# Performance work log

Hardware: AMD Instinct MI355X
Metric: run time of the kernel (lower is better)

The kernel has to match this reference:

```python
import jax, jax.numpy as jnp
import numpy as np

N, E, IN_DIM, HID, HEADS, LAYERS, NUM_STORES = 50000, 800000, 64, 128, 16, 3, 50
DH = HID // HEADS  # per-head dim = 8
EPS = 1e-5


def setup_inputs() -> dict:
    key = jax.random.key(0)
    ks = iter(jax.random.split(key, 40))
    def nrm(shape, scale):
        return jax.random.normal(next(ks), shape, dtype=jnp.float32) * scale
    inp = {}
    inp['x'] = jax.random.normal(next(ks), (N, IN_DIM), dtype=jnp.float32)
    inp['edge_index'] = jax.random.randint(next(ks), (2, E), 0, N, dtype=jnp.int32)
    inp['edge_weight'] = jax.random.uniform(next(ks), (E, 1), dtype=jnp.float32)
    inp['store_mask'] = jax.random.randint(next(ks), (N,), 0, NUM_STORES, dtype=jnp.int32)
    # input_proj: Linear + GELU + LayerNorm
    inp['in_W'] = nrm((IN_DIM, HID), IN_DIM ** -0.5)
    inp['in_b'] = jnp.zeros((HID,), jnp.float32)
    inp['in_g'] = jnp.ones((HID,), jnp.float32)
    inp['in_beta'] = jnp.zeros((HID,), jnp.float32)
    # 3 stacked GATv2 layers (stacked leading dim = layer)
    s = HID ** -0.5
    inp['gat_Wl'] = nrm((LAYERS, HID, HID), s)
    inp['gat_bl'] = jnp.zeros((LAYERS, HID), jnp.float32)
    inp['gat_Wr'] = nrm((LAYERS, HID, HID), s)
    inp['gat_br'] = jnp.zeros((LAYERS, HID), jnp.float32)
    inp['gat_We'] = nrm((LAYERS, 1, HID), 1.0)
    inp['gat_att'] = nrm((LAYERS, HEADS, DH), DH ** -0.5)
    inp['gat_bias'] = jnp.zeros((LAYERS, HID), jnp.float32)
    inp['blk_g'] = jnp.ones((LAYERS, HID), jnp.float32)
    inp['blk_b'] = jnp.zeros((LAYERS, HID), jnp.float32)
    # per-store context gate + final norm
    inp['ctx_W'] = nrm((HID, HID), s)
    inp['ctx_b'] = jnp.zeros((HID,), jnp.float32)
    inp['fin_g'] = jnp.ones((HID,), jnp.float32)
    inp['fin_b'] = jnp.zeros((HID,), jnp.float32)
    return inp


def layernorm(x, g, b):
    mu = jnp.mean(x, axis=-1, keepdims=True)
    v = jnp.mean((x - mu) ** 2, axis=-1, keepdims=True)
    return (x - mu) * jax.lax.rsqrt(v + EPS) * g + b


def gatv2_layer(x, src, dst, ea, Wl, bl, Wr, br, We, att, bias):
    # x: [N, HID]; src/dst: [Et]; ea: [Et, 1]
    n = x.shape[0]
    xl = (x @ Wl + bl).reshape(n, HEADS, DH)   # source transform
    xr = (x @ Wr + br).reshape(n, HEADS, DH)   # target transform
    ee = (ea @ We).reshape(-1, HEADS, DH)      # edge-attr embedding
    e = jax.nn.leaky_relu(xl[src] + xr[dst] + ee, 0.2)  # [Et, H, D]
    logit = jnp.einsum('ehd,hd->eh', e, att)             # [Et, H]
    # segment softmax over incoming edges of each target node
    mx = jax.ops.segment_max(logit, dst, num_segments=n)
    p = jnp.exp(logit - mx[dst])
    Z = jax.ops.segment_sum(p, dst, num_segments=n)
    alpha = p / (Z[dst] + 1e-16)
    msg = alpha[:, :, None] * xl[src]                    # [Et, H, D]
    agg = jax.ops.segment_sum(msg, dst, num_segments=n)  # [N, H, D]
    return agg.reshape(n, HEADS * DH) + bias


def forward(x, edge_index, edge_weight, store_mask, in_W, in_b, in_g, in_beta,
            gat_Wl, gat_bl, gat_Wr, gat_br, gat_We, gat_att, gat_bias,
            blk_g, blk_b, ctx_W, ctx_b, fin_g, fin_b):
    n = x.shape[0]
    h = layernorm(jax.nn.gelu(x @ in_W + in_b, approximate=False), in_g, in_beta)
    src, dst = edge_index[0], edge_index[1]
    # PyG add_self_loops with fill_value='mean': per-target mean of incoming edge attrs
    deg = jax.ops.segment_sum(jnp.ones(src.shape, h.dtype), dst, num_segments=n)
    loop_attr = jax.ops.segment_sum(edge_weight, dst, num_segments=n) / jnp.maximum(deg, 1.0)[:, None]
    loops = jnp.arange(n, dtype=src.dtype)
    srcf = jnp.concatenate([src, loops])
    dstf = jnp.concatenate([dst, loops])
    eaf = jnp.concatenate([edge_weight, loop_attr], axis=0)
    for l in range(LAYERS):  # residual block: post-norm residual around conv
        m = gatv2_layer(h, srcf, dstf, eaf, gat_Wl[l], gat_bl[l], gat_Wr[l], gat_br[l],
                        gat_We[l], gat_att[l], gat_bias[l])
        h = layernorm(h + m, blk_g[l], blk_b[l])
    # per-store segmented mean -> sigmoid gate -> scatter back
    cnt = jax.ops.segment_sum(jnp.ones((n,), h.dtype), store_mask, num_segments=NUM_STORES)
    means = jax.ops.segment_sum(h, store_mask, num_segments=NUM_STORES) / jnp.maximum(cnt, 1.0)[:, None]
    gate = jax.nn.sigmoid(means @ ctx_W + ctx_b)
    h = h + (gate * means)[store_mask]
    return layernorm(h, fin_g, fin_b)


def reference(x, edge_index, edge_weight, store_mask, in_W, in_b, in_g, in_beta,
              gat_Wl, gat_bl, gat_Wr, gat_br, gat_We, gat_att, gat_bias,
              blk_g, blk_b, ctx_W, ctx_b, fin_g, fin_b):
    return forward(x, edge_index, edge_weight, store_mask, in_W, in_b, in_g, in_beta,
                   gat_Wl, gat_bl, gat_Wr, gat_br, gat_We, gat_att, gat_bias,
                   blk_g, blk_b, ctx_W, ctx_b, fin_g, fin_b)
```

## Files before the change

kernel.cpp:

```cpp
#include <hip/hip_runtime.h>
#include <math.h>

#define NN 50000
#define EE 800000
#define ET (EE + NN)
#define HID 128
#define NSTORE 50
#define NBL 196
#define CVT_B 12500
#define CNT_B 3125
#define SCT_B 3321
#define GEMB 391
#define SSB 512

typedef unsigned short ushort_t;
typedef unsigned long long u64;
typedef __attribute__((ext_vector_type(8))) short bf8;
typedef __attribute__((ext_vector_type(4))) float f4;
typedef __attribute__((ext_vector_type(4))) unsigned int u4;

__device__ __forceinline__ float b2f(ushort_t u) {
    union { unsigned int i; float f; } v; v.i = ((unsigned int)u) << 16; return v.f;
}
__device__ __forceinline__ ushort_t f2b(float f) {
    union { float f; unsigned int i; } v; v.f = f;
    unsigned int r = (v.i + 0x7fffu + ((v.i >> 16) & 1u)) >> 16;
    return (ushort_t)r;
}
__device__ __forceinline__ void b2f2(unsigned int u, float& lo, float& hi) {
    union { unsigned int i; float f; } a, c;
    a.i = u << 16; c.i = u & 0xffff0000u;
    lo = a.f; hi = c.f;
}
__device__ __forceinline__ unsigned int pk2(float lo, float hi) {
    return (unsigned int)f2b(lo) | ((unsigned int)f2b(hi) << 16);
}

__global__ __launch_bounds__(256) void k_build(const float* __restrict__ x, const float* __restrict__ inW,
                                               const float* __restrict__ gWl, const float* __restrict__ gWr,
                                               const int* __restrict__ ei, const float* __restrict__ ew,
                                               ushort_t* __restrict__ xb, ushort_t* __restrict__ inWt,
                                               ushort_t* __restrict__ Wlt, ushort_t* __restrict__ Wrt,
                                               u64* __restrict__ packed, int* __restrict__ rank) {
    int b = blockIdx.x, t = threadIdx.x;
    if (b < CVT_B) {
        int i = b * 256 + t;
        xb[i] = f2b(x[i]);
        if (i < 128 * 64) {
            int c = i >> 6, k = i & 63;
            inWt[i] = f2b(inW[k * 128 + c]);
        }
        if (i < 3 * 128 * 128) {
            int l = i >> 14, r = i & 16383, nn2 = r >> 7, k = r & 127;
            Wlt[i] = f2b(gWl[(size_t)l * 16384 + k * 128 + nn2]);
            Wrt[i] = f2b(gWr[(size_t)l * 16384 + k * 128 + nn2]);
        }
    } else {
        int i = (b - CVT_B) * 256 + t;
        if (i < EE) {
            int dst = ei[EE + i];
            unsigned int wfix = __float2uint_rn(ew[i] * 16777216.0f);
            u64 old = atomicAdd(&packed[dst], (1ULL << 44) | (u64)wfix);
            rank[i] = (int)(old >> 44);
        }
    }
}

__global__ __launch_bounds__(256) void k_psum(const u64* __restrict__ packed, int* __restrict__ bsum) {
    int t = threadIdx.x, bidx = blockIdx.x;
    int i = bidx * 256 + t;
    int v = (i < NN) ? (int)(packed[i] >> 44) + 1 : 0;
#pragma unroll
    for (int d = 1; d < 64; d <<= 1) v += __shfl_xor(v, d);
    __shared__ int ws4[4];
    if ((t & 63) == 0) ws4[t >> 6] = v;
    __syncthreads();
    if (t == 0) bsum[bidx] = ws4[0] + ws4[1] + ws4[2] + ws4[3];
}

__global__ __launch_bounds__(256) void k_scanb(const int* __restrict__ bsum,
                                               int* __restrict__ bbase, int* __restrict__ offs) {
    __shared__ int s[256];
    int t = threadIdx.x;
    int v = (t < NBL) ? bsum[t] : 0;
    s[t] = v;
    __syncthreads();
    for (int d = 1; d < 256; d <<= 1) {
        int u = (t >= d) ? s[t - d] : 0;
        __syncthreads();
        s[t] += u;
        __syncthreads();
    }
    if (t < NBL) bbase[t] = s[t] - v;
    if (t == 0) offs[NN] = ET;
}

__global__ __launch_bounds__(256) void k_offs(const u64* __restrict__ packed,
                                              const int* __restrict__ bbase, int* __restrict__ offs) {
    __shared__ int wsum4[4];
    int t = threadIdx.x, bidx = blockIdx.x;
    int i = bidx * 256 + t;
    int v = (i < NN) ? (int)(packed[i] >> 44) + 1 : 0;
    int lane = t & 63, w = t >> 6;
    int sc = v;
#pragma unroll
    for (int d = 1; d < 64; d <<= 1) {
        int u = __shfl_up(sc, d);
        if (lane >= d) sc += u;
    }
    if (lane == 63) wsum4[w] = sc;
    __syncthreads();
    int wo = 0;
    for (int k = 0; k < w; ++k) wo += wsum4[k];
    if (i < NN) offs[i] = bbase[bidx] + wo + sc - v;
}

__global__ __launch_bounds__(256) void k_inproj(const ushort_t* __restrict__ A,
                                                const ushort_t* __restrict__ Wt,
                                                const float* __restrict__ bias,
                                                const float* __restrict__ g,
                                                const float* __restrict__ be,
                                                float* __restrict__ h,
                                                ushort_t* __restrict__ hb) {
    const int K = 64;
    __shared__ float s1[2][128], s2[2][128];
    int lane = threadIdx.x & 63, w = threadIdx.x >> 6;
    int rw = w >> 1, cw = w & 1;
    int q = lane >> 4, l16 = lane & 15;
    int row0 = blockIdx.x * 128 + rw * 64;
    int col0 = cw * 64;
    bf8 z; for (int t = 0; t < 8; ++t) z[t] = 0;

    bf8 bfr[2][4];
#pragma unroll
    for (int kk = 0; kk < 2; ++kk)
#pragma unroll
        for (int j = 0; j < 4; ++j)
            bfr[kk][j] = *(const bf8*)(Wt + (size_t)(col0 + j * 16 + l16) * K + kk * 32 + q * 8);

    f4 acc[4][4];
#pragma unroll
    for (int i = 0; i < 4; ++i)
#pragma unroll
        for (int j = 0; j < 4; ++j) acc[i][j] = (f4)(0.f);

#pragma unroll
    for (int kk = 0; kk < 2; ++kk) {
        bf8 af[4];
#pragma unroll
        for (int i = 0; i < 4; ++i) {
            int r = row0 + i * 16 + l16;
            af[i] = (r < NN) ? *(const bf8*)(A + (size_t)r * K + kk * 32 + q * 8) : z;
        }
#pragma unroll
        for (int i = 0; i < 4; ++i)
#pragma unroll
            for (int j = 0; j < 4; ++j)
                acc[i][j] = __builtin_amdgcn_mfma_f32_16x16x32_bf16(af[i], bfr[kk][j], acc[i][j], 0, 0, 0);
    }
#pragma unroll
    for (int i = 0; i < 4; ++i) {
#pragma unroll
        for (int j = 0; j < 4; ++j) {
            float bv = bias[col0 + j * 16 + l16];
#pragma unroll
            for (int r = 0; r < 4; ++r) {
                float v = acc[i][j][r] + bv;
                v = 0.5f * v * (1.f + erff(v * 0.70710678118654752f));
                acc[i][j][r] = v;
            }
        }
    }
#pragma unroll
    for (int i = 0; i < 4; ++i) {
#pragma unroll
        for (int r = 0; r < 4; ++r) {
            float sm = acc[i][0][r] + acc[i][1][r] + acc[i][2][r] + acc[i][3][r];
            float sq = acc[i][0][r] * acc[i][0][r] + acc[i][1][r] * acc[i][1][r]
                     + acc[i][2][r] * acc[i][2][r] + acc[i][3][r] * acc[i][3][r];
#pragma unroll
            for (int k = 1; k < 16; k <<= 1) { sm += __shfl_xor(sm, k); sq += __shfl_xor(sq, k); }
            if (l16 == 0) {
                int rl = rw * 64 + i * 16 + q * 4 + r;
                s1[cw][rl] = sm; s2[cw][rl] = sq;
            }
        }
    }
    __syncthreads();
#pragma unroll
    for (int i = 0; i < 4; ++i) {
#pragma unroll
        for (int r = 0; r < 4; ++r) {
            int rl = rw * 64 + i * 16 + q * 4 + r;
            int gr = blockIdx.x * 128 + rl;
            if (gr >= NN) continue;
            float sm = s1[0][rl] + s1[1][rl];
            float sq = s2[0][rl] + s2[1][rl];
            float mu = sm * (1.f / 128.f);
            float var = sq * (1.f / 128.f) - mu * mu;
            float rinv = rsqrtf(var + 1e-5f);
#pragma unroll
            for (int j = 0; j < 4; ++j) {
                int gc = col0 + j * 16 + l16;
                float v = (acc[i][j][r] - mu) * rinv * g[gc] + be[gc];
                h[(size_t)gr * HID + gc] = v;
                hb[(size_t)gr * HID + gc] = f2b(v);
            }
        }
    }
}

__global__ __launch_bounds__(256) void k_gemm2(const ushort_t* __restrict__ A,
                                               const ushort_t* __restrict__ Wt0,
                                               const ushort_t* __restrict__ Wt1,
                                               const float* __restrict__ b0,
                                               const float* __restrict__ b1,
                                               ushort_t* __restrict__ o0,
                                               ushort_t* __restrict__ o1, int n,
                                               const int* __restrict__ ei,
                                               const float* __restrict__ ew,
                                               const int* __restrict__ offs,
                                               const u64* __restrict__ packed,
                                               const int* __restrict__ rank,
                                               int2* __restrict__ csr) {
    int bid = blockIdx.x;
    if (bid >= 2 * GEMB) {
        int i = (bid - 2 * GEMB) * 256 + threadIdx.x;
        if (i < EE) {
            int src = ei[i], dst = ei[EE + i];
            int pos = offs[dst] + rank[i];
            int2 v; v.x = src; v.y = __float_as_int(ew[i]);
            csr[pos] = v;
        } else if (i < ET) {
            int nd = i - EE;
            u64 p = packed[nd];
            int deg = (int)(p >> 44);
            float wsf = (float)(p & ((1ULL << 44) - 1)) * (1.0f / 16777216.0f);
            float la = wsf / fmaxf((float)deg, 1.0f);
            int pos = offs[nd + 1] - 1;
            int2 v; v.x = nd; v.y = __float_as_int(la);
            csr[pos] = v;
        }
        return;
    }
    const int K = 128;
    int by = (bid >= GEMB) ? 1 : 0;
    int bx = by ? bid - GEMB : bid;
    const ushort_t* Wt = by ? Wt1 : Wt0;
    const float* bias = by ? b1 : b0;
    ushort_t* outb = by ? o1 : o0;
    int lane = threadIdx.x & 63, w = threadIdx.x >> 6;
    int rw = w >> 1, cw = w & 1;
    int q = lane >> 4, l16 = lane & 15;
    int row0 = bx * 128 + rw * 64;
    int col0 = cw * 64;
    bf8 z; for (int t = 0; t < 8; ++t) z[t] = 0;

    bf8 bfr[4][4];
#pragma unroll
    for (int kk = 0; kk < 4; ++kk)
#pragma unroll
        for (int j = 0; j < 4; ++j)
            bfr[kk][j] = *(const bf8*)(Wt + (size_t)(col0 + j * 16 + l16) * K + kk * 32 + q * 8);

    f4 acc[4][4];
#pragma unroll
    for (int i = 0; i < 4; ++i)
#pragma unroll
        for (int j = 0; j < 4; ++j) acc[i][j] = (f4)(0.f);

#pragma unroll
    for (int kk = 0; kk < 4; ++kk) {
        bf8 af[4];
#pragma unroll
        for (int i = 0; i < 4; ++i) {
            int r = row0 + i * 16 + l16;
            af[i] = (r < n) ? *(const bf8*)(A + (size_t)r * K + kk * 32 + q * 8) : z;
        }
#pragma unroll
        for (int i = 0; i < 4; ++i)
#pragma unroll
            for (int j = 0; j < 4; ++j)
                acc[i][j] = __builtin_amdgcn_mfma_f32_16x16x32_bf16(af[i], bfr[kk][j], acc[i][j], 0, 0, 0);
    }
#pragma unroll
    for (int i = 0; i < 4; ++i) {
        int gr0 = row0 + i * 16 + q * 4;
#pragma unroll
        for (int j = 0; j < 4; ++j) {
            int gc = col0 + j * 16 + l16;
            float bv = bias[gc];
#pragma unroll
            for (int r = 0; r < 4; ++r) {
                int gr = gr0 + r;
                if (gr < n) outb[(size_t)gr * HID + gc] = f2b(acc[i][j][r] + bv);
            }
        }
    }
}

__global__ __launch_bounds__(256) void k_attn(const ushort_t* __restrict__ xl,
                                              const ushort_t* __restrict__ xr,
                                              float* __restrict__ h,
                                              ushort_t* __restrict__ hb,
                                              const int* __restrict__ offs,
                                              const int2* __restrict__ csr,
                                              const float* __restrict__ We,
                                              const float* __restrict__ att,
                                              const float* __restrict__ gbias,
                                              const float* __restrict__ g,
                                              const float* __restrict__ b) {
    int wid = (blockIdx.x * 256 + threadIdx.x) >> 6;
    int lane = threadIdx.x & 63;
    if (wid >= NN) return;
    int hd = lane & 15;
    int grp = lane >> 4;
    int dbase = hd * 8;
    size_t base = (size_t)wid * HID;

    float xr8[8], at8[8], we8[8];
    {
        u4 uxr = *(const u4*)(xr + base + dbase);
        b2f2(uxr.x, xr8[0], xr8[1]); b2f2(uxr.y, xr8[2], xr8[3]);
        b2f2(uxr.z, xr8[4], xr8[5]); b2f2(uxr.w, xr8[6], xr8[7]);
        f4 a0 = *(const f4*)(att + dbase), a1 = *(const f4*)(att + dbase + 4);
        at8[0] = a0.x; at8[1] = a0.y; at8[2] = a0.z; at8[3] = a0.w;
        at8[4] = a1.x; at8[5] = a1.y; at8[6] = a1.z; at8[7] = a1.w;
        f4 w0 = *(const f4*)(We + dbase), w1 = *(const f4*)(We + dbase + 4);
        we8[0] = w0.x; we8[1] = w0.y; we8[2] = w0.z; we8[3] = w0.w;
        we8[4] = w1.x; we8[5] = w1.y; we8[6] = w1.z; we8[7] = w1.w;
    }
    int p0 = offs[wid], p1 = offs[wid + 1];
    float Z = 0.f;
    float acc[8];
#pragma unroll
    for (int q = 0; q < 8; ++q) acc[q] = 0.f;

#define QUAD(EJ, MASKED)                                                        \
    {                                                                           \
        int ei_ = (EJ) + grp;                                                   \
        int s_ = __shfl(sv, ei_);                                               \
        float ea_ = __shfl(evl, ei_);                                           \
        bool val_ = MASKED ? (ei_ < mm) : true;                                 \
        u4 ux_ = *(const u4*)(xl + (size_t)s_ * HID + dbase);                   \
        float x_[8];                                                            \
        b2f2(ux_.x, x_[0], x_[1]); b2f2(ux_.y, x_[2], x_[3]);                   \
        b2f2(ux_.z, x_[4], x_[5]); b2f2(ux_.w, x_[6], x_[7]);                   \
        float lg_ = 0.f;                                                        \
        _Pragma("unroll")                                                       \
        for (int q_ = 0; q_ < 8; ++q_) {                                        \
            float t_ = x_[q_] + xr8[q_] + ea_ * we8[q_];                        \
            t_ = (t_ > 0.f) ? t_ : 0.2f * t_;                                   \
            lg_ = fmaf(at8[q_], t_, lg_);                                       \
        }                                                                       \
        float w_ = val_ ? __expf(lg_) : 0.f;                                    \
        Z += w_;                                                                \
        _Pragma("unroll")                                                       \
        for (int q_ = 0; q_ < 8; ++q_) acc[q_] = fmaf(w_, x_[q_], acc[q_]);     \
    }

    for (int cb = p0; cb < p1; cb += 64) {
        int mm = min(64, p1 - cb);
        int2 m2 = (lane < mm) ? csr[cb + lane] : make_int2(0, 0);
        int sv = m2.x;
        float evl = __int_as_float(m2.y);
        int j = 0;
        for (; j + 8 <= mm; j += 8) { QUAD(j, false) QUAD(j + 4, false) }
        for (; j < mm; j += 4) QUAD(j, true)
    }
#undef QUAD

    Z += __shfl_xor(Z, 16); Z += __shfl_xor(Z, 32);
#pragma unroll
    for (int q = 0; q < 8; ++q) {
        acc[q] += __shfl_xor(acc[q], 16);
        acc[q] += __shfl_xor(acc[q], 32);
    }
    float inv = 1.f / (Z + 1e-16f);

    f4 hv0 = *(const f4*)(h + base + dbase);
    f4 hv1 = *(const f4*)(h + base + dbase + 4);
    float hres[8] = {hv0.x, hv0.y, hv0.z, hv0.w, hv1.x, hv1.y, hv1.z, hv1.w};
    f4 gb0 = *(const f4*)(gbias + dbase), gb1 = *(const f4*)(gbias + dbase + 4);
    float gb8[8] = {gb0.x, gb0.y, gb0.z, gb0.w, gb1.x, gb1.y, gb1.z, gb1.w};
    float o[8], sm = 0.f, sq = 0.f;
#pragma unroll
    for (int q = 0; q < 8; ++q) {
        o[q] = acc[q] * inv + gb8[q] + hres[q];
        sm += o[q]; sq += o[q] * o[q];
    }
#pragma unroll
    for (int k = 1; k < 16; k <<= 1) { sm += __shfl_xor(sm, k); sq += __shfl_xor(sq, k); }
    float mu = sm * (1.f / 128.f);
    float var = sq * (1.f / 128.f) - mu * mu;
    float rinv = rsqrtf(var + 1e-5f);
    f4 g0 = *(const f4*)(g + dbase), g1 = *(const f4*)(g + dbase + 4);
    float g8[8] = {g0.x, g0.y, g0.z, g0.w, g1.x, g1.y, g1.z, g1.w};
    f4 b0 = *(const f4*)(b + dbase), b1 = *(const f4*)(b + dbase + 4);
    float b8[8] = {b0.x, b0.y, b0.z, b0.w, b1.x, b1.y, b1.z, b1.w};
    float v8[8];
#pragma unroll
    for (int q = 0; q < 8; ++q) v8[q] = (o[q] - mu) * rinv * g8[q] + b8[q];
    if (grp == 0) {
        f4 s0 = {v8[0], v8[1], v8[2], v8[3]};
        f4 s1 = {v8[4], v8[5], v8[6], v8[7]};
        *(f4*)(h + base + dbase) = s0;
        *(f4*)(h + base + dbase + 4) = s1;
        u4 hu;
        hu.x = pk2(v8[0], v8[1]); hu.y = pk2(v8[2], v8[3]);
        hu.z = pk2(v8[4], v8[5]); hu.w = pk2(v8[6], v8[7]);
        *(u4*)(hb + base + dbase) = hu;
    }
}

__global__ __launch_bounds__(256) void k_store_sum(const float* __restrict__ h,
                                                   const int* __restrict__ mask,
                                                   float* __restrict__ psums,
                                                   int* __restrict__ pcnts) {
    __shared__ float ls[NSTORE * HID];
    __shared__ int lc[NSTORE];
    int t = threadIdx.x, bidx = blockIdx.x;
    for (int i = t; i < NSTORE * HID; i += 256) ls[i] = 0.f;
    if (t < NSTORE) lc[t] = 0;
    __syncthreads();
    int wid = bidx * 4 + (t >> 6);
    int lane = t & 63;
    int nw = SSB * 4;
    int d0 = lane * 2;
    for (int node = wid; node < NN; node += nw) {
        int s = mask[node];
        float2 hv = *(const float2*)(h + (size_t)node * HID + d0);
        atomicAdd(&ls[s * HID + d0], hv.x);
        atomicAdd(&ls[s * HID + d0 + 1], hv.y);
        if (lane == 0) atomicAdd(&lc[s], 1);
    }
    __syncthreads();
    for (int i = t; i < NSTORE * HID; i += 256) psums[(size_t)bidx * (NSTORE * HID) + i] = ls[i];
    if (t < NSTORE) pcnts[bidx * NSTORE + t] = lc[t];
}

__global__ __launch_bounds__(256) void k_gate(const float* __restrict__ psums,
                                              const int* __restrict__ pcnts,
                                              const float* __restrict__ ctxW,
                                              const float* __restrict__ ctxb,
                                              float* __restrict__ gm) {
    __shared__ float h1[HID];
    __shared__ float mloc[HID];
    __shared__ int cw4[4];
    int s = blockIdx.x, t = threadIdx.x;
    int d = t & 127, half = t >> 7;
    float s0 = 0.f, s1 = 0.f, s2 = 0.f, s3 = 0.f;
    for (int b = half * 4; b < SSB; b += 8) {
        s0 += psums[(size_t)(b + 0) * (NSTORE * HID) + s * HID + d];
        s1 += psums[(size_t)(b + 1) * (NSTORE * HID) + s * HID + d];
        s2 += psums[(size_t)(b + 2) * (NSTORE * HID) + s * HID + d];
        s3 += psums[(size_t)(b + 3) * (NSTORE * HID) + s * HID + d];
    }
    float sum = (s0 + s1) + (s2 + s3);
    int c = pcnts[t * NSTORE + s] + pcnts[(t + 256) * NSTORE + s];
#pragma unroll
    for (int k = 1; k < 64; k <<= 1) c += __shfl_xor(c, k);
    if ((t & 63) == 0) cw4[t >> 6] = c;
    if (half) h1[d] = sum;
    __syncthreads();
    if (half == 0) {
        float tot = sum + h1[d];
        float cnt = fmaxf((float)(cw4[0] + cw4[1] + cw4[2] + cw4[3]), 1.f);
        mloc[d] = tot / cnt;
    }
    __syncthreads();
    if (half == 0) {
        float acc = ctxb[d];
        for (int j = 0; j < HID; ++j) acc += mloc[j] * ctxW[j * HID + d];
        float gate = 1.f / (1.f + __expf(-acc));
        gm[s * HID + d] = gate * mloc[d];
    }
}

__global__ __launch_bounds__(256) void k_final(const float* __restrict__ h,
                                               const int* __restrict__ mask,
                                               const float* __restrict__ gm,
                                               const float* __restrict__ g,
                                               const float* __restrict__ b,
                                               float* __restrict__ out) {
    int wid = (blockIdx.x * 256 + threadIdx.x) >> 6;
    int lane = threadIdx.x & 63;
    if (wid >= NN) return;
    size_t base = (size_t)wid * HID;
    int s = mask[wid];
    int d0 = lane * 2, d1 = d0 + 1;
    float v0 = h[base + d0] + gm[s * HID + d0];
    float v1 = h[base + d1] + gm[s * HID + d1];
    float sm = v0 + v1, sq = v0 * v0 + v1 * v1;
#pragma unroll
    for (int k = 1; k < 64; k <<= 1) { sm += __shfl_xor(sm, k); sq += __shfl_xor(sq, k); }
    float mu = sm * (1.f / 128.f);
    float var = sq * (1.f / 128.f) - mu * mu;
    float r = rsqrtf(var + 1e-5f);
    out[base + d0] = (v0 - mu) * r * g[d0] + b[d0];
    out[base + d1] = (v1 - mu) * r * g[d1] + b[d1];
}

extern "C" void kernel_launch(void* const* d_in, const int* in_sizes, int n_in,
                              void* d_out, int out_size, void* d_ws, size_t ws_size,
                              hipStream_t stream) {
    const float* x      = (const float*)d_in[0];
    const int*   ei     = (const int*)d_in[1];
    const float* ew     = (const float*)d_in[2];
    const int*   smask  = (const int*)d_in[3];
    const float* inW    = (const float*)d_in[4];
    const float* inb    = (const float*)d_in[5];
    const float* ing    = (const float*)d_in[6];
    const float* inbeta = (const float*)d_in[7];
    const float* gWl    = (const float*)d_in[8];
    const float* gbl    = (const float*)d_in[9];
    const float* gWr    = (const float*)d_in[10];
    const float* gbr    = (const float*)d_in[11];
    const float* gWe    = (const float*)d_in[12];
    const float* gatt   = (const float*)d_in[13];
    const float* gbias  = (const float*)d_in[14];
    const float* blkg   = (const float*)d_in[15];
    const float* blkb   = (const float*)d_in[16];
    const float* ctxW   = (const float*)d_in[17];
    const float* ctxb   = (const float*)d_in[18];
    const float* fing   = (const float*)d_in[19];
    const float* finb   = (const float*)d_in[20];
    float* out = (float*)d_out;

    float* ws = (float*)d_ws;
    size_t o = 0;
    float*    h      = ws + o;              o += (size_t)NN * HID;
    int2*     csr    = (int2*)(ws + o);     o += (size_t)ET * 2;
    float*    gm     = ws + o;              o += NSTORE * HID;
    int*      offs   = (int*)(ws + o);      o += 50004;
    int*      rank   = (int*)(ws + o);      o += EE;
    ushort_t* xb     = (ushort_t*)(ws + o); o += (size_t)NN * 64 / 2;
    ushort_t* hb     = (ushort_t*)(ws + o); o += (size_t)NN * HID / 2;
    ushort_t* xlb    = (ushort_t*)(ws + o); o += (size_t)NN * HID / 2;
    ushort_t* xrb    = (ushort_t*)(ws + o); o += (size_t)NN * HID / 2;
    ushort_t* inWt   = (ushort_t*)(ws + o); o += 128 * 64 / 2;
    ushort_t* Wlt    = (ushort_t*)(ws + o); o += 3 * 128 * 128 / 2;
    ushort_t* Wrt    = (ushort_t*)(ws + o); o += 3 * 128 * 128 / 2;
    int*      bsum   = (int*)(ws + o);      o += 256;
    int*      bbase  = (int*)(ws + o);      o += 256;
    float*    psums  = ws + o;              o += (size_t)SSB * NSTORE * HID;
    int*      pcnts  = (int*)(ws + o);      o += SSB * NSTORE;
    if (o & 1) ++o;
    float*    zbase  = ws + o;
    u64*      packed = (u64*)(ws + o);      o += (size_t)NN * 2;
    size_t zbytes = (size_t)(NN * 2) * 4;

    hipMemsetAsync((void*)zbase, 0, zbytes, stream);

    const int WB = NN / 4;

    k_build<<<CVT_B + CNT_B, 256, 0, stream>>>(x, inW, gWl, gWr, ei, ew,
                                               xb, inWt, Wlt, Wrt, packed, rank);
    k_psum<<<NBL, 256, 0, stream>>>(packed, bsum);
    k_scanb<<<1, 256, 0, stream>>>(bsum, bbase, offs);
    k_offs<<<NBL, 256, 0, stream>>>(packed, bbase, offs);
    k_inproj<<<GEMB, 256, 0, stream>>>(xb, inWt, inb, ing, inbeta, h, hb);

    for (int l = 0; l < 3; ++l) {
        int nb = 2 * GEMB + (l == 0 ? SCT_B : 0);
        k_gemm2<<<nb, 256, 0, stream>>>(hb, Wlt + (size_t)l * HID * HID, Wrt + (size_t)l * HID * HID,
                                        gbl + l * HID, gbr + l * HID, xlb, xrb, NN,
                                        ei, ew, offs, packed, rank, csr);
        k_attn<<<WB, 256, 0, stream>>>(xlb, xrb, h, hb, offs, csr,
                                       gWe + l * HID, gatt + l * HID, gbias + l * HID,
                                       blkg + l * HID, blkb + l * HID);
    }

    k_store_sum<<<SSB, 256, 0, stream>>>(h, smask, psums, pcnts);
    k_gate<<<NSTORE, 256, 0, stream>>>(psums, pcnts, ctxW, ctxb, gm);
    k_final<<<WB, 256, 0, stream>>>(h, smask, gm, fing, finb, out);
}
```

Before: 542.8 us.

## Fuse input projection into build kernel and pack attention math into float2

```diff
diff --git a/kernel.cpp b/kernel.cpp
--- a/kernel.cpp
+++ b/kernel.cpp
@@ -7,8 +7,8 @@
 #define HID 128
 #define NSTORE 50
 #define NBL 196
-#define CVT_B 12500
 #define CNT_B 3125
+#define WCV_B 192
 #define SCT_B 3321
 #define GEMB 391
 #define SSB 512
@@ -17,51 +17,154 @@
 typedef unsigned long long u64;
 typedef __attribute__((ext_vector_type(8))) short bf8;
 typedef __attribute__((ext_vector_type(4))) float f4;
+typedef __attribute__((ext_vector_type(2))) float f2;
 typedef __attribute__((ext_vector_type(4))) unsigned int u4;
 
-__device__ __forceinline__ float b2f(ushort_t u) {
-    union { unsigned int i; float f; } v; v.i = ((unsigned int)u) << 16; return v.f;
-}
 __device__ __forceinline__ ushort_t f2b(float f) {
     union { float f; unsigned int i; } v; v.f = f;
     unsigned int r = (v.i + 0x7fffu + ((v.i >> 16) & 1u)) >> 16;
     return (ushort_t)r;
 }
-__device__ __forceinline__ void b2f2(unsigned int u, float& lo, float& hi) {
-    union { unsigned int i; float f; } a, c;
-    a.i = u << 16; c.i = u & 0xffff0000u;
-    lo = a.f; hi = c.f;
+__device__ __forceinline__ f2 b2f2v(unsigned int u) {
+    union { unsigned int i; float f; } lo, hi;
+    lo.i = u << 16; hi.i = u & 0xffff0000u;
+    f2 r; r.x = lo.f; r.y = hi.f; return r;
 }
 __device__ __forceinline__ unsigned int pk2(float lo, float hi) {
     return (unsigned int)f2b(lo) | ((unsigned int)f2b(hi) << 16);
+}
+__device__ __forceinline__ f2 max2(f2 a, f2 b) {
+#if __has_builtin(__builtin_elementwise_max)
+    return __builtin_elementwise_max(a, b);
+#else
+    f2 r; r.x = fmaxf(a.x, b.x); r.y = fmaxf(a.y, b.y); return r;
+#endif
 }
 
 __global__ __launch_bounds__(256) void k_build(const float* __restrict__ x, const float* __restrict__ inW,
                                                const float* __restrict__ gWl, const float* __restrict__ gWr,
                                                const int* __restrict__ ei, const float* __restrict__ ew,
-                                               ushort_t* __restrict__ xb, ushort_t* __restrict__ inWt,
+                                               const float* __restrict__ inb, const float* __restrict__ ing,
+                                               const float* __restrict__ inbeta,
                                                ushort_t* __restrict__ Wlt, ushort_t* __restrict__ Wrt,
-                                               u64* __restrict__ packed, int* __restrict__ rank) {
+                                               u64* __restrict__ packed, int* __restrict__ rank,
+                                               float* __restrict__ h, ushort_t* __restrict__ hb) {
     int b = blockIdx.x, t = threadIdx.x;
-    if (b < CVT_B) {
+    if (b < CNT_B) {
         int i = b * 256 + t;
-        xb[i] = f2b(x[i]);
-        if (i < 128 * 64) {
-            int c = i >> 6, k = i & 63;
-            inWt[i] = f2b(inW[k * 128 + c]);
-        }
-        if (i < 3 * 128 * 128) {
-            int l = i >> 14, r = i & 16383, nn2 = r >> 7, k = r & 127;
-            Wlt[i] = f2b(gWl[(size_t)l * 16384 + k * 128 + nn2]);
-            Wrt[i] = f2b(gWr[(size_t)l * 16384 + k * 128 + nn2]);
-        }
-    } else {
-        int i = (b - CVT_B) * 256 + t;
-        if (i < EE) {
-            int dst = ei[EE + i];
-            unsigned int wfix = __float2uint_rn(ew[i] * 16777216.0f);
-            u64 old = atomicAdd(&packed[dst], (1ULL << 44) | (u64)wfix);
-            rank[i] = (int)(old >> 44);
+        int dst = ei[EE + i];
+        unsigned int wfix = __float2uint_rn(ew[i] * 16777216.0f);
+        u64 old = atomicAdd(&packed[dst], (1ULL << 44) | (u64)wfix);
+        rank[i] = (int)(old >> 44);
+        return;
+    }
+    if (b < CNT_B + WCV_B) {
+        int i = (b - CNT_B) * 256 + t;
+        int l = i >> 14, r = i & 16383, nn2 = r >> 7, k = r & 127;
+        Wlt[i] = f2b(gWl[(size_t)l * 16384 + k * 128 + nn2]);
+        Wrt[i] = f2b(gWr[(size_t)l * 16384 + k * 128 + nn2]);
+        return;
+    }
+    __shared__ float s1[2][128], s2[2][128];
+    int bidx = b - CNT_B - WCV_B;
+    int lane = t & 63, w = t >> 6;
+    int rw = w >> 1, cw = w & 1;
+    int q = lane >> 4, l16 = lane & 15;
+    int row0 = bidx * 128 + rw * 64;
+    int col0 = cw * 64;
+
+    bf8 bfr[2][4];
+#pragma unroll
+    for (int kk = 0; kk < 2; ++kk)
+#pragma unroll
+        for (int j = 0; j < 4; ++j) {
+            int col = col0 + j * 16 + l16;
+            int k0 = kk * 32 + q * 8;
+            bf8 f;
+#pragma unroll
+            for (int e = 0; e < 8; ++e) f[e] = (short)f2b(inW[(size_t)(k0 + e) * HID + col]);
+            bfr[kk][j] = f;
+        }
+
+    f4 acc[4][4];
+#pragma unroll
+    for (int i = 0; i < 4; ++i)
+#pragma unroll
+        for (int j = 0; j < 4; ++j) acc[i][j] = (f4)(0.f);
+
+#pragma unroll
+    for (int kk = 0; kk < 2; ++kk) {
+        bf8 af[4];
+#pragma unroll
+        for (int i = 0; i < 4; ++i) {
+            int r = row0 + i * 16 + l16;
+            bf8 f;
+            if (r < NN) {
+                const float* xp = x + (size_t)r * 64 + kk * 32 + q * 8;
+                f4 lo = *(const f4*)xp, hi = *(const f4*)(xp + 4);
+                f[0] = (short)f2b(lo.x); f[1] = (short)f2b(lo.y);
+                f[2] = (short)f2b(lo.z); f[3] = (short)f2b(lo.w);
+                f[4] = (short)f2b(hi.x); f[5] = (short)f2b(hi.y);
+                f[6] = (short)f2b(hi.z); f[7] = (short)f2b(hi.w);
+            } else {
+                for (int e = 0; e < 8; ++e) f[e] = 0;
+            }
+            af[i] = f;
+        }
+#pragma unroll
+        for (int i = 0; i < 4; ++i)
+#pragma unroll
+            for (int j = 0; j < 4; ++j)
+                acc[i][j] = __builtin_amdgcn_mfma_f32_16x16x32_bf16(af[i], bfr[kk][j], acc[i][j], 0, 0, 0);
+    }
+#pragma unroll
+    for (int i = 0; i < 4; ++i) {
+#pragma unroll
+        for (int j = 0; j < 4; ++j) {
+            float bv = inb[col0 + j * 16 + l16];
+#pragma unroll
+            for (int r = 0; r < 4; ++r) {
+                float v = acc[i][j][r] + bv;
+                v = 0.5f * v * (1.f + erff(v * 0.70710678118654752f));
+                acc[i][j][r] = v;
+            }
+        }
+    }
+#pragma unroll
+    for (int i = 0; i < 4; ++i) {
+#pragma unroll
+        for (int r = 0; r < 4; ++r) {
+            float sm = acc[i][0][r] + acc[i][1][r] + acc[i][2][r] + acc[i][3][r];
+            float sq = acc[i][0][r] * acc[i][0][r] + acc[i][1][r] * acc[i][1][r]
+                     + acc[i][2][r] * acc[i][2][r] + acc[i][3][r] * acc[i][3][r];
+#pragma unroll
+            for (int k = 1; k < 16; k <<= 1) { sm += __shfl_xor(sm, k); sq += __shfl_xor(sq, k); }
+            if (l16 == 0) {
+                int rl = rw * 64 + i * 16 + q * 4 + r;
+                s1[cw][rl] = sm; s2[cw][rl] = sq;
+            }
+        }
+    }
+    __syncthreads();
+#pragma unroll
+    for (int i = 0; i < 4; ++i) {
+#pragma unroll
+        for (int r = 0; r < 4; ++r) {
+            int rl = rw * 64 + i * 16 + q * 4 + r;
+            int gr = bidx * 128 + rl;
+            if (gr >= NN) continue;
+            float sm = s1[0][rl] + s1[1][rl];
+            float sq = s2[0][rl] + s2[1][rl];
+            float mu = sm * (1.f / 128.f);
+            float var = sq * (1.f / 128.f) - mu * mu;
+            float rinv = rsqrtf(var + 1e-5f);
+#pragma unroll
+            for (int j = 0; j < 4; ++j) {
+                int gc = col0 + j * 16 + l16;
+                float v = (acc[i][j][r] - mu) * rinv * ing[gc] + inbeta[gc];
+                h[(size_t)gr * HID + gc] = v;
+                hb[(size_t)gr * HID + gc] = f2b(v);
+            }
         }
     }
 }
@@ -113,101 +216,6 @@
     int wo = 0;
     for (int k = 0; k < w; ++k) wo += wsum4[k];
     if (i < NN) offs[i] = bbase[bidx] + wo + sc - v;
-}
-
-__global__ __launch_bounds__(256) void k_inproj(const ushort_t* __restrict__ A,
-                                                const ushort_t* __restrict__ Wt,
-                                                const float* __restrict__ bias,
-                                                const float* __restrict__ g,
-                                                const float* __restrict__ be,
-                                                float* __restrict__ h,
-                                                ushort_t* __restrict__ hb) {
-    const int K = 64;
-    __shared__ float s1[2][128], s2[2][128];
-    int lane = threadIdx.x & 63, w = threadIdx.x >> 6;
-    int rw = w >> 1, cw = w & 1;
-    int q = lane >> 4, l16 = lane & 15;
-    int row0 = blockIdx.x * 128 + rw * 64;
-    int col0 = cw * 64;
-    bf8 z; for (int t = 0; t < 8; ++t) z[t] = 0;
-
-    bf8 bfr[2][4];
-#pragma unroll
-    for (int kk = 0; kk < 2; ++kk)
-#pragma unroll
-        for (int j = 0; j < 4; ++j)
-            bfr[kk][j] = *(const bf8*)(Wt + (size_t)(col0 + j * 16 + l16) * K + kk * 32 + q * 8);
-
-    f4 acc[4][4];
-#pragma unroll
-    for (int i = 0; i < 4; ++i)
-#pragma unroll
-        for (int j = 0; j < 4; ++j) acc[i][j] = (f4)(0.f);
-
-#pragma unroll
-    for (int kk = 0; kk < 2; ++kk) {
-        bf8 af[4];
-#pragma unroll
-        for (int i = 0; i < 4; ++i) {
-            int r = row0 + i * 16 + l16;
-            af[i] = (r < NN) ? *(const bf8*)(A + (size_t)r * K + kk * 32 + q * 8) : z;
-        }
-#pragma unroll
-        for (int i = 0; i < 4; ++i)
-#pragma unroll
-            for (int j = 0; j < 4; ++j)
-                acc[i][j] = __builtin_amdgcn_mfma_f32_16x16x32_bf16(af[i], bfr[kk][j], acc[i][j], 0, 0, 0);
-    }
-#pragma unroll
-    for (int i = 0; i < 4; ++i) {
-#pragma unroll
-        for (int j = 0; j < 4; ++j) {
-            float bv = bias[col0 + j * 16 + l16];
-#pragma unroll
-            for (int r = 0; r < 4; ++r) {
-                float v = acc[i][j][r] + bv;
-                v = 0.5f * v * (1.f + erff(v * 0.70710678118654752f));
-                acc[i][j][r] = v;
-            }
-        }
-    }
-#pragma unroll
-    for (int i = 0; i < 4; ++i) {
-#pragma unroll
-        for (int r = 0; r < 4; ++r) {
-            float sm = acc[i][0][r] + acc[i][1][r] + acc[i][2][r] + acc[i][3][r];
-            float sq = acc[i][0][r] * acc[i][0][r] + acc[i][1][r] * acc[i][1][r]
-                     + acc[i][2][r] * acc[i][2][r] + acc[i][3][r] * acc[i][3][r];
-#pragma unroll
-            for (int k = 1; k < 16; k <<= 1) { sm += __shfl_xor(sm, k); sq += __shfl_xor(sq, k); }
-            if (l16 == 0) {
-                int rl = rw * 64 + i * 16 + q * 4 + r;
-                s1[cw][rl] = sm; s2[cw][rl] = sq;
-            }
-        }
-    }
-    __syncthreads();
-#pragma unroll
-    for (int i = 0; i < 4; ++i) {
-#pragma unroll
-        for (int r = 0; r < 4; ++r) {
-            int rl = rw * 64 + i * 16 + q * 4 + r;
-            int gr = blockIdx.x * 128 + rl;
-            if (gr >= NN) continue;
-            float sm = s1[0][rl] + s1[1][rl];
-            float sq = s2[0][rl] + s2[1][rl];
-            float mu = sm * (1.f / 128.f);
-            float var = sq * (1.f / 128.f) - mu * mu;
-            float rinv = rsqrtf(var + 1e-5f);
-#pragma unroll
-            for (int j = 0; j < 4; ++j) {
-                int gc = col0 + j * 16 + l16;
-                float v = (acc[i][j][r] - mu) * rinv * g[gc] + be[gc];
-                h[(size_t)gr * HID + gc] = v;
-                hb[(size_t)gr * HID + gc] = f2b(v);
-            }
-        }
-    }
 }
 
 __global__ __launch_bounds__(256) void k_gemm2(const ushort_t* __restrict__ A,
@@ -318,23 +326,23 @@
     int dbase = hd * 8;
     size_t base = (size_t)wid * HID;
 
-    float xr8[8], at8[8], we8[8];
+    f2 xr2[4], at2[4], we2[4];
     {
         u4 uxr = *(const u4*)(xr + base + dbase);
-        b2f2(uxr.x, xr8[0], xr8[1]); b2f2(uxr.y, xr8[2], xr8[3]);
-        b2f2(uxr.z, xr8[4], xr8[5]); b2f2(uxr.w, xr8[6], xr8[7]);
+        xr2[0] = b2f2v(uxr.x); xr2[1] = b2f2v(uxr.y);
+        xr2[2] = b2f2v(uxr.z); xr2[3] = b2f2v(uxr.w);
         f4 a0 = *(const f4*)(att + dbase), a1 = *(const f4*)(att + dbase + 4);
-        at8[0] = a0.x; at8[1] = a0.y; at8[2] = a0.z; at8[3] = a0.w;
-        at8[4] = a1.x; at8[5] = a1.y; at8[6] = a1.z; at8[7] = a1.w;
+        at2[0].x = a0.x; at2[0].y = a0.y; at2[1].x = a0.z; at2[1].y = a0.w;
+        at2[2].x = a1.x; at2[2].y = a1.y; at2[3].x = a1.z; at2[3].y = a1.w;
         f4 w0 = *(const f4*)(We + dbase), w1 = *(const f4*)(We + dbase + 4);
-        we8[0] = w0.x; we8[1] = w0.y; we8[2] = w0.z; we8[3] = w0.w;
-        we8[4] = w1.x; we8[5] = w1.y; we8[6] = w1.z; we8[7] = w1.w;
+        we2[0].x = w0.x; we2[0].y = w0.y; we2[1].x = w0.z; we2[1].y = w0.w;
+        we2[2].x = w1.x; we2[2].y = w1.y; we2[3].x = w1.z; we2[3].y = w1.w;
     }
     int p0 = offs[wid], p1 = offs[wid + 1];
     float Z = 0.f;
-    float acc[8];
-#pragma unroll
-    for (int q = 0; q < 8; ++q) acc[q] = 0.f;
+    f2 acc2[4];
+#pragma unroll
+    for (int q = 0; q < 4; ++q) { acc2[q].x = 0.f; acc2[q].y = 0.f; }
 
 #define QUAD(EJ, MASKED)                                                        \
     {                                                                           \
@@ -343,20 +351,20 @@
         float ea_ = __shfl(evl, ei_);                                           \
         bool val_ = MASKED ? (ei_ < mm) : true;                                 \
         u4 ux_ = *(const u4*)(xl + (size_t)s_ * HID + dbase);                   \
-        float x_[8];                                                            \
-        b2f2(ux_.x, x_[0], x_[1]); b2f2(ux_.y, x_[2], x_[3]);                   \
-        b2f2(ux_.z, x_[4], x_[5]); b2f2(ux_.w, x_[6], x_[7]);                   \
-        float lg_ = 0.f;                                                        \
+        f2 x2_[4];                                                              \
+        x2_[0] = b2f2v(ux_.x); x2_[1] = b2f2v(ux_.y);                           \
+        x2_[2] = b2f2v(ux_.z); x2_[3] = b2f2v(ux_.w);                           \
+        f2 lg2_; lg2_.x = 0.f; lg2_.y = 0.f;                                    \
         _Pragma("unroll")                                                       \
-        for (int q_ = 0; q_ < 8; ++q_) {                                        \
-            float t_ = x_[q_] + xr8[q_] + ea_ * we8[q_];                        \
-            t_ = (t_ > 0.f) ? t_ : 0.2f * t_;                                   \
-            lg_ = fmaf(at8[q_], t_, lg_);                                       \
+        for (int q_ = 0; q_ < 4; ++q_) {                                        \
+            f2 t_ = (x2_[q_] + xr2[q_]) + ea_ * we2[q_];                        \
+            t_ = max2(t_, t_ * 0.2f);                                           \
+            lg2_ += at2[q_] * t_;                                               \
         }                                                                       \
-        float w_ = val_ ? __expf(lg_) : 0.f;                                    \
+        float w_ = val_ ? __expf(lg2_.x + lg2_.y) : 0.f;                        \
         Z += w_;                                                                \
         _Pragma("unroll")                                                       \
-        for (int q_ = 0; q_ < 8; ++q_) acc[q_] = fmaf(w_, x_[q_], acc[q_]);     \
+        for (int q_ = 0; q_ < 4; ++q_) acc2[q_] += w_ * x2_[q_];                \
     }
 
     for (int cb = p0; cb < p1; cb += 64) {
@@ -372,11 +380,15 @@
 
     Z += __shfl_xor(Z, 16); Z += __shfl_xor(Z, 32);
 #pragma unroll
-    for (int q = 0; q < 8; ++q) {
-        acc[q] += __shfl_xor(acc[q], 16);
-        acc[q] += __shfl_xor(acc[q], 32);
+    for (int q = 0; q < 4; ++q) {
+        acc2[q].x += __shfl_xor(acc2[q].x, 16);
+        acc2[q].x += __shfl_xor(acc2[q].x, 32);
+        acc2[q].y += __shfl_xor(acc2[q].y, 16);
+        acc2[q].y += __shfl_xor(acc2[q].y, 32);
     }
     float inv = 1.f / (Z + 1e-16f);
+    float acc[8] = {acc2[0].x, acc2[0].y, acc2[1].x, acc2[1].y,
+                    acc2[2].x, acc2[2].y, acc2[3].x, acc2[3].y};
 
     f4 hv0 = *(const f4*)(h + base + dbase);
     f4 hv1 = *(const f4*)(h + base + dbase + 4);
@@ -534,11 +546,9 @@
     float*    gm     = ws + o;              o += NSTORE * HID;
     int*      offs   = (int*)(ws + o);      o += 50004;
     int*      rank   = (int*)(ws + o);      o += EE;
-    ushort_t* xb     = (ushort_t*)(ws + o); o += (size_t)NN * 64 / 2;
     ushort_t* hb     = (ushort_t*)(ws + o); o += (size_t)NN * HID / 2;
     ushort_t* xlb    = (ushort_t*)(ws + o); o += (size_t)NN * HID / 2;
     ushort_t* xrb    = (ushort_t*)(ws + o); o += (size_t)NN * HID / 2;
-    ushort_t* inWt   = (ushort_t*)(ws + o); o += 128 * 64 / 2;
     ushort_t* Wlt    = (ushort_t*)(ws + o); o += 3 * 128 * 128 / 2;
     ushort_t* Wrt    = (ushort_t*)(ws + o); o += 3 * 128 * 128 / 2;
     int*      bsum   = (int*)(ws + o);      o += 256;
@@ -554,12 +564,12 @@
 
     const int WB = NN / 4;
 
-    k_build<<<CVT_B + CNT_B, 256, 0, stream>>>(x, inW, gWl, gWr, ei, ew,
-                                               xb, inWt, Wlt, Wrt, packed, rank);
+    k_build<<<CNT_B + WCV_B + GEMB, 256, 0, stream>>>(x, inW, gWl, gWr, ei, ew,
+                                                      inb, ing, inbeta,
+                                                      Wlt, Wrt, packed, rank, h, hb);
     k_psum<<<NBL, 256, 0, stream>>>(packed, bsum);
     k_scanb<<<1, 256, 0, stream>>>(bsum, bbase, offs);
     k_offs<<<NBL, 256, 0, stream>>>(packed, bbase, offs);
-    k_inproj<<<GEMB, 256, 0, stream>>>(xb, inWt, inb, ing, inbeta, h, hb);
 
     for (int l = 0; l < 3; ++l) {
         int nb = 2 * GEMB + (l == 0 ? SCT_B : 0);
```

Result: faster. 518.5 us (-4.5%).
